# Kernel tuning notes

Measured on AMD Instinct MI355X. Metric: run time of the kernel, lower is better.

The kernel has to match this reference:

```python
import jax, jax.numpy as jnp
import numpy as np

B, S, D = 32, 128, 1024      # encoder batch, seq len, embed_dim
C = 65536                    # nclasses (sense inventory)
N = 512                      # number of gathered WSD target tokens
NNZ = 262144                 # nnz of sparse label adjacency A (avg degree 4)
EPS = 1e-5                   # BatchNorm1d eps


def setup_inputs() -> dict:
    key = jax.random.key(0)
    ks = jax.random.split(key, 7)
    enc_out = jax.random.normal(ks[0], (B, S, D), dtype=jnp.float32)
    batch_idx = jax.random.randint(ks[1], (N,), 0, B)
    tgt = jax.random.randint(ks[2], (N,), 0, S)
    A_indices = jax.random.randint(ks[3], (2, NNZ), 0, C)
    A_values = jax.random.uniform(ks[4], (NNZ,), dtype=jnp.float32)
    wt2_w = jax.random.normal(ks[5], (C, D), dtype=jnp.float32) / np.sqrt(D).astype(np.float32)
    wt2_b = jax.random.normal(ks[6], (C,), dtype=jnp.float32) * 0.02
    return {"enc_out": enc_out, "wt2_w": wt2_w, "wt2_b": wt2_b,
            "A_values": A_values, "batch_idx": batch_idx, "tgt": tgt,
            "A_indices": A_indices}


def reference(enc_out, wt2_w, wt2_b, A_values, batch_idx, tgt, A_indices):
    # gather target-token embeddings: [N, D]
    g = enc_out[batch_idx, tgt]
    # BatchNorm1d(affine=False), training mode -> batch stats, biased var
    mean = jnp.mean(g, axis=0)
    var = jnp.var(g, axis=0)
    h0 = (g - mean) / jnp.sqrt(var + EPS)
    # wt2 Linear + swish -> logits over classes Z: [N, C]
    h1 = jax.nn.swish(h0 @ wt2_w.T + wt2_b)
    # sparse spmm: torch_sparse.spmm(ii, vv, m=C, n=C, matrix=Z.T).T == Z @ A.T
    row, col = A_indices[0], A_indices[1]
    gathered = h1.T[col] * A_values[:, None]            # [NNZ, N]
    neighbors = jax.ops.segment_sum(gathered, row, num_segments=C).T  # [N, C]
    # residual add (renormalize=False)
    return neighbors + h1
```

## Files before the change

kernel.cpp:

```cpp
#include <hip/hip_runtime.h>
#include <hip/hip_bf16.h>

typedef unsigned short u16;
typedef unsigned int   u32;
typedef __attribute__((ext_vector_type(8))) short bf16x8;
typedef __attribute__((ext_vector_type(4))) float f32x4;

static constexpr int kS = 128, kD = 1024, kC = 65536, kN = 512, kNNZ = 262144;

__device__ __forceinline__ u16 f2bf(float x) {
  u32 u = __float_as_uint(x);
  u32 r = (u + 0x7fffu + ((u >> 16) & 1u)) >> 16;
  return (u16)r;
}
__device__ __forceinline__ u32 pack2(float a, float b) {
  return (u32)f2bf(a) | ((u32)f2bf(b) << 16);
}
__device__ __forceinline__ float bf_lo(u32 v) { return __uint_as_float(v << 16); }
__device__ __forceinline__ float bf_hi(u32 v) { return __uint_as_float(v & 0xffff0000u); }

__global__ void k_bn_part(const float* __restrict__ enc, const int* __restrict__ bidx,
                          const int* __restrict__ tgt, float* __restrict__ part) {
  __shared__ int offs[64];
  int n0 = blockIdx.y * 64;
  if (threadIdx.x < 64) offs[threadIdx.x] = bidx[n0 + threadIdx.x] * kS + tgt[n0 + threadIdx.x];
  __syncthreads();
  int d = blockIdx.x * 256 + threadIdx.x;
  float s = 0.f, ss = 0.f;
  for (int i = 0; i < 64; ++i) {
    float v = enc[(size_t)offs[i] * kD + d];
    s += v; ss += v * v;
  }
  part[(blockIdx.y * 2 + 0) * kD + d] = s;
  part[(blockIdx.y * 2 + 1) * kD + d] = ss;
}

__global__ void k_bn_fin(const float* __restrict__ part, float* __restrict__ mean,
                         float* __restrict__ rstd) {
  int d = blockIdx.x * 256 + threadIdx.x;
  float s = 0.f, ss = 0.f;
#pragma unroll
  for (int b = 0; b < 8; ++b) {
    s  += part[(b * 2 + 0) * kD + d];
    ss += part[(b * 2 + 1) * kD + d];
  }
  float m = s * (1.f / kN);
  float var = ss * (1.f / kN) - m * m;
  mean[d] = m;
  rstd[d] = 1.f / sqrtf(var + 1e-5f);
}

__global__ void k_bn_pack(const float* __restrict__ enc, const int* __restrict__ bidx,
                          const int* __restrict__ tgt, const float* __restrict__ mean,
                          const float* __restrict__ rstd, u16* __restrict__ Bp) {
  int i = blockIdx.x * 256 + threadIdx.x;
  int n = i & 511;
  int g = i >> 9;
  int k0 = g * 8;
  size_t src = (size_t)(bidx[n] * kS + tgt[n]) * kD + k0;
  float4 v0 = *(const float4*)(enc + src);
  float4 v1 = *(const float4*)(enc + src + 4);
  float4 m0 = *(const float4*)(mean + k0);
  float4 m1 = *(const float4*)(mean + k0 + 4);
  float4 r0 = *(const float4*)(rstd + k0);
  float4 r1 = *(const float4*)(rstd + k0 + 4);
  u32 q0 = pack2((v0.x - m0.x) * r0.x, (v0.y - m0.y) * r0.y);
  u32 q1 = pack2((v0.z - m0.z) * r0.z, (v0.w - m0.w) * r0.w);
  u32 q2 = pack2((v1.x - m1.x) * r1.x, (v1.y - m1.y) * r1.y);
  u32 q3 = pack2((v1.z - m1.z) * r1.z, (v1.w - m1.w) * r1.w);
  *(uint4*)(Bp + (size_t)i * 8) = make_uint4(q0, q1, q2, q3);
}

__global__ void k_hist(const int* __restrict__ rows, int* __restrict__ hist) {
  int e = blockIdx.x * blockDim.x + threadIdx.x;
  if (e < kNNZ) atomicAdd(&hist[rows[e]], 1);
}

__global__ __launch_bounds__(1024) void k_scan(int* __restrict__ hist, int* __restrict__ cursor) {
  __shared__ int sm[1024];
  int t = threadIdx.x;
  int base = t * 64;
  int sum = 0;
  for (int i = 0; i < 64; ++i) sum += hist[base + i];
  sm[t] = sum;
  __syncthreads();
  for (int off = 1; off < 1024; off <<= 1) {
    int v = (t >= off) ? sm[t - off] : 0;
    __syncthreads();
    sm[t] += v;
    __syncthreads();
  }
  int run = sm[t] - sum;
  for (int i = 0; i < 64; ++i) {
    int v = hist[base + i];
    hist[base + i] = run;
    cursor[base + i] = run;
    run += v;
  }
  if (t == 1023) hist[kC] = run;
}

__global__ void k_scatter(const int* __restrict__ rows, const int* __restrict__ cols,
                          const float* __restrict__ vals, int* __restrict__ cursor,
                          int* __restrict__ scol, float* __restrict__ sval) {
  int e = blockIdx.x * blockDim.x + threadIdx.x;
  if (e < kNNZ) {
    int r = rows[e];
    int p = atomicAdd(&cursor[r], 1);
    scol[p] = cols[e];
    sval[p] = vals[e];
  }
}

__global__ __launch_bounds__(512, 4)
void k_gemm_f3(const float* __restrict__ W, const u16* __restrict__ Bp,
               const float* __restrict__ bias, u16* __restrict__ h1t) {
  __shared__ __align__(16) u16 Ab0[64 * 36];
  __shared__ __align__(16) u16 Ab1[64 * 36];
  const int t = threadIdx.x;
  const int l = t & 63;
  const int w = t >> 6;
  const int wn = w * 64;
  const int cb = blockIdx.x * 64;
  const int ar = t >> 3, aq = t & 7;
  const int q = l >> 4, ln = l & 15;
  const float* gA = W + (size_t)(cb + ar) * kD + aq * 4;
  u16* awp0 = Ab0 + ar * 36 + aq * 4;
  u16* awp1 = Ab1 + ar * 36 + aq * 4;
  const u16* gB = Bp + ((size_t)q * 512 + wn + ln) * 8;

  f32x4 acc[4][4];
#pragma unroll
  for (int a = 0; a < 4; ++a)
#pragma unroll
    for (int b = 0; b < 4; ++b) acc[a][b] = (f32x4){0.f, 0.f, 0.f, 0.f};

  float4 fA;
  bf16x8 bvA[4], bvB[4];

  fA = *(const float4*)(gA);
#pragma unroll
  for (int nb = 0; nb < 4; ++nb) bvA[nb] = *(const bf16x8*)(gB + nb * 128);
  *(uint2*)awp0 = make_uint2(pack2(fA.x, fA.y), pack2(fA.z, fA.w));
  fA = *(const float4*)(gA + 32);
#pragma unroll
  for (int nb = 0; nb < 4; ++nb) bvB[nb] = *(const bf16x8*)(gB + 16384 + nb * 128);
  asm volatile("s_waitcnt lgkmcnt(0)" ::: "memory");
  __builtin_amdgcn_s_barrier();
  __builtin_amdgcn_sched_barrier(0);

#pragma unroll 1
  for (int tt = 0; tt < 16; ++tt) {
    {
#pragma unroll
      for (int mb = 0; mb < 4; ++mb) {
        bf16x8 af = *(const bf16x8*)(Ab0 + (mb * 16 + ln) * 36 + q * 8);
#pragma unroll
        for (int nb = 0; nb < 4; ++nb)
          acc[mb][nb] = __builtin_amdgcn_mfma_f32_16x16x32_bf16(af, bvA[nb], acc[mb][nb], 0, 0, 0);
      }
      *(uint2*)awp1 = make_uint2(pack2(fA.x, fA.y), pack2(fA.z, fA.w));
      int ktn = (2 * tt + 2) & 31;
      fA = *(const float4*)(gA + ktn * 32);
#pragma unroll
      for (int nb = 0; nb < 4; ++nb)
        bvA[nb] = *(const bf16x8*)(gB + (size_t)ktn * 16384 + nb * 128);
      asm volatile("s_waitcnt lgkmcnt(0)" ::: "memory");
      __builtin_amdgcn_s_barrier();
      __builtin_amdgcn_sched_barrier(0);
    }
    {
#pragma unroll
      for (int mb = 0; mb < 4; ++mb) {
        bf16x8 af = *(const bf16x8*)(Ab1 + (mb * 16 + ln) * 36 + q * 8);
#pragma unroll
        for (int nb = 0; nb < 4; ++nb)
          acc[mb][nb] = __builtin_amdgcn_mfma_f32_16x16x32_bf16(af, bvB[nb], acc[mb][nb], 0, 0, 0);
      }
      if (tt < 15) {
        *(uint2*)awp0 = make_uint2(pack2(fA.x, fA.y), pack2(fA.z, fA.w));
        int ktn = 2 * tt + 3;
        fA = *(const float4*)(gA + ktn * 32);
#pragma unroll
        for (int nb = 0; nb < 4; ++nb)
          bvB[nb] = *(const bf16x8*)(gB + (size_t)ktn * 16384 + nb * 128);
        asm volatile("s_waitcnt lgkmcnt(0)" ::: "memory");
        __builtin_amdgcn_s_barrier();
        __builtin_amdgcn_sched_barrier(0);
      }
    }
  }

#pragma unroll
  for (int mb = 0; mb < 4; ++mb) {
    int rb = mb * 16 + q * 4;
#pragma unroll
    for (int i = 0; i < 4; ++i) {
      int c = cb + rb + i;
      float bvs = bias[c];
#pragma unroll
      for (int nb = 0; nb < 4; ++nb) {
        float x = acc[mb][nb][i] + bvs;
        float sw = x / (1.f + __expf(-x));
        h1t[(size_t)c * kN + (wn + nb * 16 + ln)] = f2bf(sw);
      }
    }
  }
}

#define FMA8(cv, v)                                                        \
  a0 = fmaf(v, bf_lo(cv.x), a0); a1 = fmaf(v, bf_hi(cv.x), a1);            \
  a2 = fmaf(v, bf_lo(cv.y), a2); a3 = fmaf(v, bf_hi(cv.y), a3);            \
  a4 = fmaf(v, bf_lo(cv.z), a4); a5 = fmaf(v, bf_hi(cv.z), a5);            \
  a6 = fmaf(v, bf_lo(cv.w), a6); a7 = fmaf(v, bf_hi(cv.w), a7);

__global__ __launch_bounds__(512)
void k_spmm(const u16* __restrict__ h1t, const int* __restrict__ rowptr,
            const int* __restrict__ scol, const float* __restrict__ sval,
            float* __restrict__ out) {
  __shared__ float tile[32 * 512];
  int r0 = blockIdx.x * 32;
  int t = threadIdx.x, w = t >> 6, l = t & 63;
#pragma unroll
  for (int j = 0; j < 4; ++j) {
    int rl = w * 4 + j;
    int r = r0 + rl;
    uint4 hv = ((const uint4*)(h1t + (size_t)r * kN))[l];
    float a0 = bf_lo(hv.x), a1 = bf_hi(hv.x), a2 = bf_lo(hv.y), a3 = bf_hi(hv.y);
    float a4 = bf_lo(hv.z), a5 = bf_hi(hv.z), a6 = bf_lo(hv.w), a7 = bf_hi(hv.w);
    int e0 = rowptr[r], e1 = rowptr[r + 1];
    uint4 cv0 = {}, cv1 = {};
    float v0 = 0.f, v1 = 0.f;
    if (e0 < e1) {
      v0 = sval[e0];
      cv0 = ((const uint4*)(h1t + (size_t)scol[e0] * kN))[l];
    }
    if (e0 + 1 < e1) {
      v1 = sval[e0 + 1];
      cv1 = ((const uint4*)(h1t + (size_t)scol[e0 + 1] * kN))[l];
    }
    for (int e = e0; e < e1; e += 2) {
      FMA8(cv0, v0);
      if (e + 2 < e1) {
        v0 = sval[e + 2];
        cv0 = ((const uint4*)(h1t + (size_t)scol[e + 2] * kN))[l];
      }
      if (e + 1 < e1) {
        FMA8(cv1, v1);
        if (e + 3 < e1) {
          v1 = sval[e + 3];
          cv1 = ((const uint4*)(h1t + (size_t)scol[e + 3] * kN))[l];
        }
      }
    }
    int sw = (rl & 7) << 2;
    *(float4*)&tile[rl * 512 + ((8 * l) ^ sw)]     = make_float4(a0, a1, a2, a3);
    *(float4*)&tile[rl * 512 + ((8 * l + 4) ^ sw)] = make_float4(a4, a5, a6, a7);
  }
  __syncthreads();
  int r = l & 31;
  int swr = (r & 7) << 2;
#pragma unroll
  for (int it = 0; it < 32; ++it) {
    int n = it * 16 + w * 2 + (l >> 5);
    out[(size_t)n * kC + r0 + r] = tile[r * 512 + (n ^ swr)];
  }
}

extern "C" void kernel_launch(void* const* d_in, const int* in_sizes, int n_in,
                              void* d_out, int out_size, void* d_ws, size_t ws_size,
                              hipStream_t stream) {
  (void)in_sizes; (void)n_in; (void)out_size; (void)ws_size;
  const float* enc   = (const float*)d_in[0];
  const float* W     = (const float*)d_in[1];
  const float* bias  = (const float*)d_in[2];
  const float* Avals = (const float*)d_in[3];
  const int*   bidx  = (const int*)d_in[4];
  const int*   tgt   = (const int*)d_in[5];
  const int*   Arow  = (const int*)d_in[6];
  const int*   Acol  = Arow + kNNZ;
  float* out = (float*)d_out;

  char* ws = (char*)d_ws;
  float* mean   = (float*)(ws);
  float* rstd   = (float*)(ws + 4096);
  u16*   Bp     = (u16*)  (ws + 8192);
  int*   rowptr = (int*)  (ws + 1056768);
  int*   cursor = (int*)  (ws + 1319168);
  int*   scol   = (int*)  (ws + 1581312);
  float* sval   = (float*)(ws + 2629888);
  float* part   = (float*)(ws + 3678464);
  u16*   h1t    = (u16*)  (ws + 4194304);

  hipMemsetAsync(rowptr, 0, (kC + 1) * sizeof(int), stream);
  k_bn_part<<<dim3(4, 8), 256, 0, stream>>>(enc, bidx, tgt, part);
  k_bn_fin<<<4, 256, 0, stream>>>(part, mean, rstd);
  k_bn_pack<<<256, 256, 0, stream>>>(enc, bidx, tgt, mean, rstd, Bp);
  k_hist<<<kNNZ / 256, 256, 0, stream>>>(Arow, rowptr);
  k_scan<<<1, 1024, 0, stream>>>(rowptr, cursor);
  k_scatter<<<kNNZ / 256, 256, 0, stream>>>(Arow, Acol, Avals, cursor, scol, sval);
  k_gemm_f3<<<kC / 64, 512, 0, stream>>>(W, Bp, bias, h1t);
  k_spmm<<<kC / 32, 512, 0, stream>>>(h1t, rowptr, scol, sval, out);
}
```

Measured before the change: 292.9 us.

## Stream fp32 W tiles into swizzled LDS via global_load_lds, convert at fragment load

The GEMM now copies fp32 weight tiles (64x64 per stage) straight from global memory into LDS with async global_load_lds. The stores use an XOR-swizzled layout to avoid bank conflicts, and fp32-to-bf16 packing moves to the fragment read. The B operand is now loaded from global per k-substep rather than prefetched into registers a stage ahead. This is meant to cut register staging and VALU conversion on the load path and to overlap W fetch with MFMA. In exchange it uses twice the LDS, repeats conversions per wave, and exposes B load latency. The prologue writes g1 at Ab1-16384+s1*16, which lands s1's data in Ab0's upper half, so the addressing relies on Ab1 sitting directly after Ab0 in LDS.

```diff
diff --git a/kernel.cpp b/kernel.cpp
--- a/kernel.cpp
+++ b/kernel.cpp
@@ -18,6 +18,12 @@
 }
 __device__ __forceinline__ float bf_lo(u32 v) { return __uint_as_float(v << 16); }
 __device__ __forceinline__ float bf_hi(u32 v) { return __uint_as_float(v & 0xffff0000u); }
+
+__device__ __forceinline__ void gload16(const void* g, void* l) {
+  __builtin_amdgcn_global_load_lds(
+      (const __attribute__((address_space(1))) void*)g,
+      (__attribute__((address_space(3))) void*)l, 16, 0, 0);
+}
 
 __global__ void k_bn_part(const float* __restrict__ enc, const int* __restrict__ bidx,
                           const int* __restrict__ tgt, float* __restrict__ part) {
@@ -113,21 +119,24 @@
 }
 
 __global__ __launch_bounds__(512, 4)
-void k_gemm_f3(const float* __restrict__ W, const u16* __restrict__ Bp,
+void k_gemm_f4(const float* __restrict__ W, const u16* __restrict__ Bp,
                const float* __restrict__ bias, u16* __restrict__ h1t) {
-  __shared__ __align__(16) u16 Ab0[64 * 36];
-  __shared__ __align__(16) u16 Ab1[64 * 36];
+  __shared__ __align__(16) float Ab0[64 * 64];
+  __shared__ __align__(16) float Ab1[64 * 64];
   const int t = threadIdx.x;
   const int l = t & 63;
   const int w = t >> 6;
   const int wn = w * 64;
   const int cb = blockIdx.x * 64;
-  const int ar = t >> 3, aq = t & 7;
   const int q = l >> 4, ln = l & 15;
-  const float* gA = W + (size_t)(cb + ar) * kD + aq * 4;
-  u16* awp0 = Ab0 + ar * 36 + aq * 4;
-  u16* awp1 = Ab1 + ar * 36 + aq * 4;
-  const u16* gB = Bp + ((size_t)q * 512 + wn + ln) * 8;
+
+  const int s0 = t, s1 = t + 512;
+  const int r0s = s0 >> 4, c0 = (s0 & 15) ^ (r0s & 7);
+  const int r1s = s1 >> 4, c1 = (s1 & 15) ^ (r1s & 7);
+  const float* g0 = W + (size_t)(cb + r0s) * kD + c0 * 4;
+  const float* g1 = W + (size_t)(cb + r1s) * kD + c1 * 4;
+
+  const u16* gB = Bp + (size_t)q * 4096 + (size_t)(wn + ln) * 8;
 
   f32x4 acc[4][4];
 #pragma unroll
@@ -135,60 +144,43 @@
 #pragma unroll
     for (int b = 0; b < 4; ++b) acc[a][b] = (f32x4){0.f, 0.f, 0.f, 0.f};
 
-  float4 fA;
-  bf16x8 bvA[4], bvB[4];
-
-  fA = *(const float4*)(gA);
-#pragma unroll
-  for (int nb = 0; nb < 4; ++nb) bvA[nb] = *(const bf16x8*)(gB + nb * 128);
-  *(uint2*)awp0 = make_uint2(pack2(fA.x, fA.y), pack2(fA.z, fA.w));
-  fA = *(const float4*)(gA + 32);
-#pragma unroll
-  for (int nb = 0; nb < 4; ++nb) bvB[nb] = *(const bf16x8*)(gB + 16384 + nb * 128);
-  asm volatile("s_waitcnt lgkmcnt(0)" ::: "memory");
-  __builtin_amdgcn_s_barrier();
-  __builtin_amdgcn_sched_barrier(0);
+  gload16(g0, (char*)Ab0 + s0 * 16);
+  gload16(g1, (char*)Ab1 - 16384 + s1 * 16);
+  __syncthreads();
 
 #pragma unroll 1
   for (int tt = 0; tt < 16; ++tt) {
-    {
+    const float* cur = (tt & 1) ? Ab1 : Ab0;
+    float* nxt = (tt & 1) ? Ab0 : Ab1;
+    if (tt < 15) {
+      size_t go = (size_t)(tt + 1) * 64;
+      gload16(g0 + go, (char*)nxt + s0 * 16);
+      gload16(g1 + go, (char*)nxt + s1 * 16);
+    }
+#pragma unroll
+    for (int ks = 0; ks < 2; ++ks) {
+      bf16x8 bv[4];
+#pragma unroll
+      for (int nb = 0; nb < 4; ++nb)
+        bv[nb] = *(const bf16x8*)(gB + (size_t)(tt * 8 + ks * 4) * 4096 + nb * 128);
 #pragma unroll
       for (int mb = 0; mb < 4; ++mb) {
-        bf16x8 af = *(const bf16x8*)(Ab0 + (mb * 16 + ln) * 36 + q * 8);
+        int rr = mb * 16 + ln;
+        int sb = ks * 8 + q * 2;
+        const char* rowp = (const char*)cur + rr * 256;
+        float4 a0 = *(const float4*)(rowp + ((sb + 0) ^ (rr & 7)) * 16);
+        float4 a1 = *(const float4*)(rowp + ((sb + 1) ^ (rr & 7)) * 16);
+        union { u32 u[4]; bf16x8 v; } cvt;
+        cvt.u[0] = pack2(a0.x, a0.y);
+        cvt.u[1] = pack2(a0.z, a0.w);
+        cvt.u[2] = pack2(a1.x, a1.y);
+        cvt.u[3] = pack2(a1.z, a1.w);
 #pragma unroll
         for (int nb = 0; nb < 4; ++nb)
-          acc[mb][nb] = __builtin_amdgcn_mfma_f32_16x16x32_bf16(af, bvA[nb], acc[mb][nb], 0, 0, 0);
-      }
-      *(uint2*)awp1 = make_uint2(pack2(fA.x, fA.y), pack2(fA.z, fA.w));
-      int ktn = (2 * tt + 2) & 31;
-      fA = *(const float4*)(gA + ktn * 32);
-#pragma unroll
-      for (int nb = 0; nb < 4; ++nb)
-        bvA[nb] = *(const bf16x8*)(gB + (size_t)ktn * 16384 + nb * 128);
-      asm volatile("s_waitcnt lgkmcnt(0)" ::: "memory");
-      __builtin_amdgcn_s_barrier();
-      __builtin_amdgcn_sched_barrier(0);
-    }
-    {
-#pragma unroll
-      for (int mb = 0; mb < 4; ++mb) {
-        bf16x8 af = *(const bf16x8*)(Ab1 + (mb * 16 + ln) * 36 + q * 8);
-#pragma unroll
-        for (int nb = 0; nb < 4; ++nb)
-          acc[mb][nb] = __builtin_amdgcn_mfma_f32_16x16x32_bf16(af, bvB[nb], acc[mb][nb], 0, 0, 0);
-      }
-      if (tt < 15) {
-        *(uint2*)awp0 = make_uint2(pack2(fA.x, fA.y), pack2(fA.z, fA.w));
-        int ktn = 2 * tt + 3;
-        fA = *(const float4*)(gA + ktn * 32);
-#pragma unroll
-        for (int nb = 0; nb < 4; ++nb)
-          bvB[nb] = *(const bf16x8*)(gB + (size_t)ktn * 16384 + nb * 128);
-        asm volatile("s_waitcnt lgkmcnt(0)" ::: "memory");
-        __builtin_amdgcn_s_barrier();
-        __builtin_amdgcn_sched_barrier(0);
-      }
-    }
+          acc[mb][nb] = __builtin_amdgcn_mfma_f32_16x16x32_bf16(cvt.v, bv[nb], acc[mb][nb], 0, 0, 0);
+      }
+    }
+    __syncthreads();
   }
 
 #pragma unroll
@@ -299,6 +291,6 @@
   k_hist<<<kNNZ / 256, 256, 0, stream>>>(Arow, rowptr);
   k_scan<<<1, 1024, 0, stream>>>(rowptr, cursor);
   k_scatter<<<kNNZ / 256, 256, 0, stream>>>(Arow, Acol, Avals, cursor, scol, sval);
-  k_gemm_f3<<<kC / 64, 512, 0, stream>>>(W, Bp, bias, h1t);
+  k_gemm_f4<<<kC / 64, 512, 0, stream>>>(W, Bp, bias, h1t);
   k_spmm<<<kC / 32, 512, 0, stream>>>(h1t, rowptr, scol, sval, out);
 }
```

Measured after the change: 299.3 us. +2.2%, slower.
